# Kernel optimization log

Hardware: AMD Instinct MI355X
Metric: run time of the kernel (lower is better)

The kernel has to match this reference:

```python
import jax, jax.numpy as jnp
import numpy as np

CTX_WIN = 5
PAD = (CTX_WIN - 1) // 2


def setup_inputs() -> dict:
    key = jax.random.key(0)
    k1, k2, k3 = jax.random.split(key, 3)
    B, S, H, A = 64, 1024, 128, 8
    return {
        "batch_docIn": jax.random.normal(k1, (B, S, H), dtype=jnp.float32),
        "aspEmbed_weight": jax.random.uniform(k2, (A, CTX_WIN * H), dtype=jnp.float32, minval=-0.01, maxval=0.01),
        "aspProj": jax.random.uniform(k3, (A, H, H), dtype=jnp.float32, minval=-0.01, maxval=0.01),
    }


def reference(batch_docIn, aspEmbed_weight, aspProj):
    B, S, H = batch_docIn.shape
    A = aspProj.shape[0]
    # Per-aspect projection: (A, B, S, H)
    proj = jnp.einsum('bsh,ahf->absf', batch_docIn, aspProj)
    E = aspEmbed_weight.reshape(A, H, CTX_WIN)
    # Zero-pad along seq, then accumulate windowed scores without materializing
    padded = jnp.pad(proj, ((0, 0), (0, 0), (PAD, PAD), (0, 0)))
    attn = sum(
        jnp.einsum('absh,ah->abs',
                   jax.lax.dynamic_slice_in_dim(padded, w, S, axis=2),
                   E[:, :, w])
        for w in range(CTX_WIN)
    )  # (A, B, S)
    attn = jax.nn.softmax(attn, axis=2)  # softmax over seq (torch dim=1)
    rep = jnp.einsum('absh,abs->abh', proj, attn)  # (A, B, H)
    # outputs: attn (B, A, S), rep (B, A, H)
    return attn.transpose(1, 0, 2), rep.transpose(1, 0, 2)
```

## Files before the change

kernel.cpp:

```cpp
#include <hip/hip_runtime.h>
#include <hip/hip_bf16.h>

#define S_DIM 1024
#define H_DIM 128
#define A_DIM 8
#define W_WIN 5

typedef unsigned int uint;
typedef unsigned short ushort;
typedef __attribute__((ext_vector_type(8))) short short8;
typedef __attribute__((ext_vector_type(4))) float f32x4;

union U128 { uint4 u; short8 s; };

__device__ __forceinline__ ushort f2bf(float f) {
    uint u = __float_as_uint(f);
    uint r = (u + 0x7fffu + ((u >> 16) & 1u)) >> 16;
    return (ushort)r;
}

__global__ __launch_bounds__(128) void k_g(const float* __restrict__ P,
                                           const float* __restrict__ We,
                                           ushort* __restrict__ Gt) {
    const int a = blockIdx.x;
    const int h = threadIdx.x;
    if (a >= A_DIM) {
        for (int i = h; i < W_WIN * H_DIM; i += 128) Gt[a * (W_WIN * H_DIM) + i] = 0;
        return;
    }
    __shared__ float Es[H_DIM * W_WIN];
    for (int i = h; i < H_DIM * W_WIN; i += 128) Es[i] = We[a * (H_DIM * W_WIN) + i];
    __syncthreads();

    const float* Pr = P + ((size_t)a * H_DIM + h) * H_DIM;
    float acc[W_WIN] = {0.f, 0.f, 0.f, 0.f, 0.f};
#pragma unroll 8
    for (int f = 0; f < H_DIM; f += 4) {
        float4 pv = *(const float4*)(Pr + f);
        float pj[4] = {pv.x, pv.y, pv.z, pv.w};
#pragma unroll
        for (int j = 0; j < 4; ++j) {
            const float p = pj[j];
            const float* e = &Es[(f + j) * W_WIN];
#pragma unroll
            for (int w = 0; w < W_WIN; ++w) acc[w] += p * e[w];
        }
    }
#pragma unroll
    for (int w = 0; w < W_WIN; ++w)
        Gt[a * (W_WIN * H_DIM) + w * H_DIM + h] = f2bf(acc[w]);
}

#define CS 128
#define RROWS (CS + 4)
#define GPAD 81
#define EPITCH 136
__global__ __launch_bounds__(256) void k_scores(const float* __restrict__ Din,
                                                const ushort* __restrict__ Gt,
                                                float* __restrict__ escore,
                                                float* __restrict__ numPart,
                                                float* __restrict__ Zpart) {
    __shared__ uint4 Dl[RROWS * 16];
    __shared__ uint4 Gl[16 * GPAD];
    __shared__ ushort el[16 * EPITCH];
    __shared__ float Zw[32];
    const int b   = blockIdx.y;
    const int slc = blockIdx.x;
    const int s0  = slc * CS;
    const int t   = threadIdx.x;
    const float* Db = Din + (size_t)b * S_DIM * H_DIM;

    for (int i = t; i < RROWS * 16; i += 256) {
        const int r = i >> 4, c = i & 15;
        const int gs = s0 - 2 + r;
        float4 va = make_float4(0.f, 0.f, 0.f, 0.f), vb = va;
        if (gs >= 0 && gs < S_DIM) {
            const float* p = Db + (size_t)gs * H_DIM + c * 8;
            va = ((const float4*)p)[0];
            vb = ((const float4*)p)[1];
        }
        uint4 q;
        q.x = (uint)f2bf(va.x) | ((uint)f2bf(va.y) << 16);
        q.y = (uint)f2bf(va.z) | ((uint)f2bf(va.w) << 16);
        q.z = (uint)f2bf(vb.x) | ((uint)f2bf(vb.y) << 16);
        q.w = (uint)f2bf(vb.z) | ((uint)f2bf(vb.w) << 16);
        Dl[r * 16 + (c ^ (r & 15))] = q;
    }
    {
        const uint4* Gg = (const uint4*)Gt;
        for (int i = t; i < 16 * 80; i += 256) {
            const int n = i / 80, c = i - n * 80;
            Gl[n * GPAD + c] = Gg[i];
        }
    }
    __syncthreads();

    const int lane = t & 63;
    const int wv   = t >> 6;
    const int lm   = lane & 15;
    const int lq   = lane >> 4;

    f32x4 acc0 = {0.f, 0.f, 0.f, 0.f};
    f32x4 acc1 = {0.f, 0.f, 0.f, 0.f};
#pragma unroll
    for (int kk = 0; kk < 20; ++kk) {
        const int w = kk >> 2;
        const int r0 = wv * 16 + lm + w;
        const int cidx = (kk & 3) * 4 + lq;
        const int cx = cidx ^ (r0 & 15);
        U128 av0, av1, bv;
        bv.u  = Gl[lm * GPAD + kk * 4 + lq];
        av0.u = Dl[r0 * 16 + cx];
        av1.u = Dl[(r0 + 64) * 16 + cx];
        acc0 = __builtin_amdgcn_mfma_f32_16x16x32_bf16(av0.s, bv.s, acc0, 0, 0, 0);
        acc1 = __builtin_amdgcn_mfma_f32_16x16x32_bf16(av1.s, bv.s, acc1, 0, 0, 0);
    }

    float4 e0, e1;
    e0.x = __expf(acc0.x); e0.y = __expf(acc0.y); e0.z = __expf(acc0.z); e0.w = __expf(acc0.w);
    e1.x = __expf(acc1.x); e1.y = __expf(acc1.y); e1.z = __expf(acc1.z); e1.w = __expf(acc1.w);

    if (lm < A_DIM) {
        float* op = escore + (((size_t)b * A_DIM + lm) * S_DIM) + s0 + wv * 16 + lq * 4;
        *(float4*)op = e0;
        *(float4*)(op + 64) = e1;
    }
    {
        const int sb = wv * 16 + lq * 4;
        uint2 d0, d1;
        d0.x = (uint)f2bf(e0.x) | ((uint)f2bf(e0.y) << 16);
        d0.y = (uint)f2bf(e0.z) | ((uint)f2bf(e0.w) << 16);
        d1.x = (uint)f2bf(e1.x) | ((uint)f2bf(e1.y) << 16);
        d1.y = (uint)f2bf(e1.z) | ((uint)f2bf(e1.w) << 16);
        *(uint2*)(&el[lm * EPITCH + sb])      = d0;
        *(uint2*)(&el[lm * EPITCH + sb + 64]) = d1;
    }
    float es = e0.x + e0.y + e0.z + e0.w + e1.x + e1.y + e1.z + e1.w;
    es += __shfl_xor(es, 16);
    es += __shfl_xor(es, 32);
    if (lq == 0 && lm < A_DIM) Zw[wv * 8 + lm] = es;
    __syncthreads();

    const ushort* Dls = (const ushort*)Dl;
    U128 afr[4];
#pragma unroll
    for (int kk = 0; kk < 4; ++kk)
        afr[kk].u = *(const uint4*)(&el[lm * EPITCH + kk * 32 + lq * 8]);

    f32x4 accN[2] = {{0.f,0.f,0.f,0.f},{0.f,0.f,0.f,0.f}};
#pragma unroll
    for (int nt = 0; nt < 2; ++nt) {
        const int h  = (wv * 2 + nt) * 16 + lm;
        const int ch = h >> 3, hw = h & 7;
#pragma unroll
        for (int kk = 0; kk < 4; ++kk) {
            uint p[4];
#pragma unroll
            for (int jj = 0; jj < 4; ++jj) {
                const int sj = kk * 32 + lq * 8 + jj * 2;
                const int ra = sj + 2, rb = sj + 3;
                const uint lo = Dls[(ra * 16 + (ch ^ (ra & 15))) * 8 + hw];
                const uint hi = Dls[(rb * 16 + (ch ^ (rb & 15))) * 8 + hw];
                p[jj] = lo | (hi << 16);
            }
            U128 bfr; bfr.u = make_uint4(p[0], p[1], p[2], p[3]);
            accN[nt] = __builtin_amdgcn_mfma_f32_16x16x32_bf16(afr[kk].s, bfr.s, accN[nt], 0, 0, 0);
        }
    }

    if (lq < 2) {
#pragma unroll
        for (int nt = 0; nt < 2; ++nt) {
            const int h = (wv * 2 + nt) * 16 + lm;
#pragma unroll
            for (int r = 0; r < 4; ++r)
                numPart[(((size_t)(b * 8 + slc) * 8) + lq * 4 + r) * H_DIM + h] = accN[nt][r];
        }
    }
    if (t < A_DIM)
        Zpart[(b * 8 + slc) * 8 + t] = Zw[t] + Zw[8 + t] + Zw[16 + t] + Zw[24 + t];
}

__global__ __launch_bounds__(128) void k_final(const float* __restrict__ escore,
                                               const float* __restrict__ numPart,
                                               const float* __restrict__ Zpart,
                                               const float* __restrict__ P,
                                               float* __restrict__ attn,
                                               float* __restrict__ rep) {
    __shared__ float ws[H_DIM];
    const int ba = blockIdx.x;
    const int b = ba >> 3, a = ba & 7;
    const int t = threadIdx.x;

    float Zs = 0.f;
#pragma unroll
    for (int k = 0; k < 8; ++k) Zs += Zpart[(b * 8 + k) * 8 + a];
    const float rz = 1.0f / Zs;

    float s = 0.f;
#pragma unroll
    for (int k = 0; k < 8; ++k)
        s += numPart[(((size_t)(b * 8 + k) * 8) + a) * H_DIM + t];
    ws[t] = s * rz;

    const float* ep = escore + (size_t)ba * S_DIM;
    float* ap = attn + (size_t)ba * S_DIM;
#pragma unroll
    for (int i = 0; i < 2; ++i) {
        float4 v = *(const float4*)(ep + i * 512 + t * 4);
        v.x *= rz; v.y *= rz; v.z *= rz; v.w *= rz;
        *(float4*)(ap + i * 512 + t * 4) = v;
    }
    __syncthreads();

    const float* Pa = P + (size_t)a * H_DIM * H_DIM + t;
    float acc = 0.f;
#pragma unroll 32
    for (int hh = 0; hh < H_DIM; ++hh)
        acc += ws[hh] * Pa[(size_t)hh * H_DIM];
    rep[(size_t)ba * H_DIM + t] = acc;
}

extern "C" void kernel_launch(void* const* d_in, const int* in_sizes, int n_in,
                              void* d_out, int out_size, void* d_ws, size_t ws_size,
                              hipStream_t stream) {
    const float* docIn = (const float*)d_in[0];
    const float* We    = (const float*)d_in[1];
    const float* P     = (const float*)d_in[2];
    float* out = (float*)d_out;

    const int B = in_sizes[0] / (S_DIM * H_DIM);

    ushort* Gt     = (ushort*)d_ws;
    float* escore  = (float*)((char*)d_ws + 32768);
    float* numPart = escore + (size_t)B * A_DIM * S_DIM;
    float* Zpart   = numPart + (size_t)B * 8 * A_DIM * H_DIM;

    k_g<<<16, 128, 0, stream>>>(P, We, Gt);
    k_scores<<<dim3(S_DIM / CS, B), 256, 0, stream>>>(docIn, Gt, escore, numPart, Zpart);
    k_final<<<B * A_DIM, 128, 0, stream>>>(escore, numPart, Zpart, P, out,
                                           out + (size_t)B * A_DIM * S_DIM);
}
```

Measured before the change: 91.94 us.

## Fuse final normalization and projection into scores kernel via last-block atomics

Result: slower. 112.2 us (+22.0%).

```diff
diff --git a/kernel.cpp b/kernel.cpp
--- a/kernel.cpp
+++ b/kernel.cpp
@@ -21,9 +21,21 @@
 
 __global__ __launch_bounds__(128) void k_g(const float* __restrict__ P,
                                            const float* __restrict__ We,
-                                           ushort* __restrict__ Gt) {
+                                           ushort* __restrict__ Gt,
+                                           float* __restrict__ numAcc,
+                                           float* __restrict__ Z,
+                                           uint* __restrict__ cnt) {
     const int a = blockIdx.x;
     const int h = threadIdx.x;
+
+    {
+        float4 z4 = make_float4(0.f, 0.f, 0.f, 0.f);
+        float4* np = (float4*)(numAcc + (size_t)a * 4096);
+        for (int i = h; i < 1024; i += 128) np[i] = z4;
+        if (a == 0) for (int i = h; i < 64 * A_DIM; i += 128) Z[i] = 0.f;
+        if (a == 1 && h < 64) cnt[h] = 0u;
+    }
+
     if (a >= A_DIM) {
         for (int i = h; i < W_WIN * H_DIM; i += 128) Gt[a * (W_WIN * H_DIM) + i] = 0;
         return;
@@ -55,15 +67,20 @@
 #define RROWS (CS + 4)
 #define GPAD 81
 #define EPITCH 136
-__global__ __launch_bounds__(256) void k_scores(const float* __restrict__ Din,
-                                                const ushort* __restrict__ Gt,
-                                                float* __restrict__ escore,
-                                                float* __restrict__ numPart,
-                                                float* __restrict__ Zpart) {
+__global__ __launch_bounds__(256) void k_fused(const float* __restrict__ Din,
+                                               const ushort* __restrict__ Gt,
+                                               const float* __restrict__ P,
+                                               float* __restrict__ escore,
+                                               float* __restrict__ numAcc,
+                                               float* __restrict__ Z,
+                                               uint* __restrict__ cnt,
+                                               float* __restrict__ attn,
+                                               float* __restrict__ rep) {
     __shared__ uint4 Dl[RROWS * 16];
     __shared__ uint4 Gl[16 * GPAD];
     __shared__ ushort el[16 * EPITCH];
     __shared__ float Zw[32];
+    __shared__ int lastFlag;
     const int b   = blockIdx.y;
     const int slc = blockIdx.x;
     const int s0  = slc * CS;
@@ -174,51 +191,52 @@
             const int h = (wv * 2 + nt) * 16 + lm;
 #pragma unroll
             for (int r = 0; r < 4; ++r)
-                numPart[(((size_t)(b * 8 + slc) * 8) + lq * 4 + r) * H_DIM + h] = accN[nt][r];
+                atomicAdd(&numAcc[((size_t)(b * 8 + lq * 4 + r)) * H_DIM + h], accN[nt][r]);
         }
     }
     if (t < A_DIM)
-        Zpart[(b * 8 + slc) * 8 + t] = Zw[t] + Zw[8 + t] + Zw[16 + t] + Zw[24 + t];
-}
-
-__global__ __launch_bounds__(128) void k_final(const float* __restrict__ escore,
-                                               const float* __restrict__ numPart,
-                                               const float* __restrict__ Zpart,
-                                               const float* __restrict__ P,
-                                               float* __restrict__ attn,
-                                               float* __restrict__ rep) {
-    __shared__ float ws[H_DIM];
-    const int ba = blockIdx.x;
-    const int b = ba >> 3, a = ba & 7;
-    const int t = threadIdx.x;
-
-    float Zs = 0.f;
-#pragma unroll
-    for (int k = 0; k < 8; ++k) Zs += Zpart[(b * 8 + k) * 8 + a];
-    const float rz = 1.0f / Zs;
-
-    float s = 0.f;
-#pragma unroll
-    for (int k = 0; k < 8; ++k)
-        s += numPart[(((size_t)(b * 8 + k) * 8) + a) * H_DIM + t];
-    ws[t] = s * rz;
-
-    const float* ep = escore + (size_t)ba * S_DIM;
-    float* ap = attn + (size_t)ba * S_DIM;
-#pragma unroll
-    for (int i = 0; i < 2; ++i) {
-        float4 v = *(const float4*)(ep + i * 512 + t * 4);
+        atomicAdd(&Z[b * A_DIM + t], Zw[t] + Zw[8 + t] + Zw[16 + t] + Zw[24 + t]);
+    __syncthreads();
+
+    if (t == 0) {
+        __threadfence();
+        lastFlag = (atomicAdd(&cnt[b], 1u) == 7u);
+    }
+    __syncthreads();
+    if (!lastFlag) return;
+    __threadfence();
+
+    float* wsl = (float*)Gl;
+    float* Zf  = wsl + 1024;
+    if (t < A_DIM) Zf[t] = 1.0f / Z[b * A_DIM + t];
+    __syncthreads();
+
+#pragma unroll
+    for (int i = 0; i < 4; ++i) {
+        const int idx = t + 256 * i;
+        wsl[idx] = numAcc[(size_t)b * 8 * H_DIM + idx] * Zf[idx >> 7];
+    }
+#pragma unroll
+    for (int a = 0; a < A_DIM; ++a) {
+        const size_t off = ((size_t)b * A_DIM + a) * S_DIM + t * 4;
+        float4 v = *(const float4*)(escore + off);
+        const float rz = Zf[a];
         v.x *= rz; v.y *= rz; v.z *= rz; v.w *= rz;
-        *(float4*)(ap + i * 512 + t * 4) = v;
-    }
-    __syncthreads();
-
-    const float* Pa = P + (size_t)a * H_DIM * H_DIM + t;
-    float acc = 0.f;
+        *(float4*)(attn + off) = v;
+    }
+    __syncthreads();
+#pragma unroll
+    for (int i = 0; i < 4; ++i) {
+        const int idx = t + 256 * i;
+        const int a = idx >> 7, f = idx & 127;
+        const float* Pa = P + ((size_t)a * H_DIM) * H_DIM + f;
+        const float* wa = wsl + a * H_DIM;
+        float acc = 0.f;
 #pragma unroll 32
-    for (int hh = 0; hh < H_DIM; ++hh)
-        acc += ws[hh] * Pa[(size_t)hh * H_DIM];
-    rep[(size_t)ba * H_DIM + t] = acc;
+        for (int hh = 0; hh < H_DIM; ++hh)
+            acc += wa[hh] * Pa[(size_t)hh * H_DIM];
+        rep[(size_t)b * A_DIM * H_DIM + idx] = acc;
+    }
 }
 
 extern "C" void kernel_launch(void* const* d_in, const int* in_sizes, int n_in,
@@ -233,11 +251,12 @@
 
     ushort* Gt     = (ushort*)d_ws;
     float* escore  = (float*)((char*)d_ws + 32768);
-    float* numPart = escore + (size_t)B * A_DIM * S_DIM;
-    float* Zpart   = numPart + (size_t)B * 8 * A_DIM * H_DIM;
-
-    k_g<<<16, 128, 0, stream>>>(P, We, Gt);
-    k_scores<<<dim3(S_DIM / CS, B), 256, 0, stream>>>(docIn, Gt, escore, numPart, Zpart);
-    k_final<<<B * A_DIM, 128, 0, stream>>>(escore, numPart, Zpart, P, out,
-                                           out + (size_t)B * A_DIM * S_DIM);
-}
+    float* numAcc  = escore + (size_t)B * A_DIM * S_DIM;
+    float* Z       = numAcc + (size_t)B * A_DIM * H_DIM;
+    uint*  cnt     = (uint*)(Z + B * A_DIM);
+
+    k_g<<<16, 128, 0, stream>>>(P, We, Gt, numAcc, Z, cnt);
+    k_fused<<<dim3(S_DIM / CS, B), 256, 0, stream>>>(docIn, Gt, P, escore,
+                                                     numAcc, Z, cnt, out,
+                                                     out + (size_t)B * A_DIM * S_DIM);
+}
```

## Halve score chunk size, store exp-scores as bf16, swizzle G in LDS

Applied to the files above, without the earlier changes.

Result: no change. 92.21 us (+0.3%).

```diff
diff --git a/kernel.cpp b/kernel.cpp
--- a/kernel.cpp
+++ b/kernel.cpp
@@ -51,17 +51,16 @@
         Gt[a * (W_WIN * H_DIM) + w * H_DIM + h] = f2bf(acc[w]);
 }
 
-#define CS 128
+#define CS 64
 #define RROWS (CS + 4)
-#define GPAD 81
-#define EPITCH 136
+#define EPITCH 88
 __global__ __launch_bounds__(256) void k_scores(const float* __restrict__ Din,
                                                 const ushort* __restrict__ Gt,
-                                                float* __restrict__ escore,
+                                                ushort* __restrict__ escore,
                                                 float* __restrict__ numPart,
                                                 float* __restrict__ Zpart) {
     __shared__ uint4 Dl[RROWS * 16];
-    __shared__ uint4 Gl[16 * GPAD];
+    __shared__ uint4 Gl[16 * 80];
     __shared__ ushort el[16 * EPITCH];
     __shared__ float Zw[32];
     const int b   = blockIdx.y;
@@ -90,7 +89,7 @@
         const uint4* Gg = (const uint4*)Gt;
         for (int i = t; i < 16 * 80; i += 256) {
             const int n = i / 80, c = i - n * 80;
-            Gl[n * GPAD + c] = Gg[i];
+            Gl[n * 80 + ((c & ~15) | ((c & 15) ^ (n & 15)))] = Gg[i];
         }
     }
     __syncthreads();
@@ -101,59 +100,47 @@
     const int lq   = lane >> 4;
 
     f32x4 acc0 = {0.f, 0.f, 0.f, 0.f};
-    f32x4 acc1 = {0.f, 0.f, 0.f, 0.f};
 #pragma unroll
     for (int kk = 0; kk < 20; ++kk) {
         const int w = kk >> 2;
         const int r0 = wv * 16 + lm + w;
         const int cidx = (kk & 3) * 4 + lq;
-        const int cx = cidx ^ (r0 & 15);
-        U128 av0, av1, bv;
-        bv.u  = Gl[lm * GPAD + kk * 4 + lq];
-        av0.u = Dl[r0 * 16 + cx];
-        av1.u = Dl[(r0 + 64) * 16 + cx];
-        acc0 = __builtin_amdgcn_mfma_f32_16x16x32_bf16(av0.s, bv.s, acc0, 0, 0, 0);
-        acc1 = __builtin_amdgcn_mfma_f32_16x16x32_bf16(av1.s, bv.s, acc1, 0, 0, 0);
-    }
-
-    float4 e0, e1;
+        const int gc = kk * 4 + lq;
+        U128 av, bv;
+        bv.u = Gl[lm * 80 + ((gc & ~15) | ((gc & 15) ^ (lm & 15)))];
+        av.u = Dl[r0 * 16 + (cidx ^ (r0 & 15))];
+        acc0 = __builtin_amdgcn_mfma_f32_16x16x32_bf16(av.s, bv.s, acc0, 0, 0, 0);
+    }
+
+    float4 e0;
     e0.x = __expf(acc0.x); e0.y = __expf(acc0.y); e0.z = __expf(acc0.z); e0.w = __expf(acc0.w);
-    e1.x = __expf(acc1.x); e1.y = __expf(acc1.y); e1.z = __expf(acc1.z); e1.w = __expf(acc1.w);
-
-    if (lm < A_DIM) {
-        float* op = escore + (((size_t)b * A_DIM + lm) * S_DIM) + s0 + wv * 16 + lq * 4;
-        *(float4*)op = e0;
-        *(float4*)(op + 64) = e1;
-    }
-    {
-        const int sb = wv * 16 + lq * 4;
-        uint2 d0, d1;
-        d0.x = (uint)f2bf(e0.x) | ((uint)f2bf(e0.y) << 16);
-        d0.y = (uint)f2bf(e0.z) | ((uint)f2bf(e0.w) << 16);
-        d1.x = (uint)f2bf(e1.x) | ((uint)f2bf(e1.y) << 16);
-        d1.y = (uint)f2bf(e1.z) | ((uint)f2bf(e1.w) << 16);
-        *(uint2*)(&el[lm * EPITCH + sb])      = d0;
-        *(uint2*)(&el[lm * EPITCH + sb + 64]) = d1;
-    }
-    float es = e0.x + e0.y + e0.z + e0.w + e1.x + e1.y + e1.z + e1.w;
+    uint2 d0;
+    d0.x = (uint)f2bf(e0.x) | ((uint)f2bf(e0.y) << 16);
+    d0.y = (uint)f2bf(e0.z) | ((uint)f2bf(e0.w) << 16);
+    const int sb = wv * 16 + lq * 4;
+    if (lm < A_DIM)
+        *(uint2*)(escore + (((size_t)b * A_DIM + lm) << 10) + s0 + sb) = d0;
+    *(uint2*)(&el[lm * EPITCH + sb]) = d0;
+
+    float es = e0.x + e0.y + e0.z + e0.w;
     es += __shfl_xor(es, 16);
     es += __shfl_xor(es, 32);
     if (lq == 0 && lm < A_DIM) Zw[wv * 8 + lm] = es;
     __syncthreads();
 
     const ushort* Dls = (const ushort*)Dl;
-    U128 afr[4];
-#pragma unroll
-    for (int kk = 0; kk < 4; ++kk)
+    U128 afr[2];
+#pragma unroll
+    for (int kk = 0; kk < 2; ++kk)
         afr[kk].u = *(const uint4*)(&el[lm * EPITCH + kk * 32 + lq * 8]);
 
     f32x4 accN[2] = {{0.f,0.f,0.f,0.f},{0.f,0.f,0.f,0.f}};
 #pragma unroll
     for (int nt = 0; nt < 2; ++nt) {
-        const int h  = (wv * 2 + nt) * 16 + lm;
+        const int h  = wv * 32 + nt * 16 + lm;
         const int ch = h >> 3, hw = h & 7;
 #pragma unroll
-        for (int kk = 0; kk < 4; ++kk) {
+        for (int kk = 0; kk < 2; ++kk) {
             uint p[4];
 #pragma unroll
             for (int jj = 0; jj < 4; ++jj) {
@@ -171,17 +158,17 @@
     if (lq < 2) {
 #pragma unroll
         for (int nt = 0; nt < 2; ++nt) {
-            const int h = (wv * 2 + nt) * 16 + lm;
+            const int h = wv * 32 + nt * 16 + lm;
 #pragma unroll
             for (int r = 0; r < 4; ++r)
-                numPart[(((size_t)(b * 8 + slc) * 8) + lq * 4 + r) * H_DIM + h] = accN[nt][r];
+                numPart[(((size_t)(b * 16 + slc) * 8) + lq * 4 + r) * H_DIM + h] = accN[nt][r];
         }
     }
     if (t < A_DIM)
-        Zpart[(b * 8 + slc) * 8 + t] = Zw[t] + Zw[8 + t] + Zw[16 + t] + Zw[24 + t];
-}
-
-__global__ __launch_bounds__(128) void k_final(const float* __restrict__ escore,
+        Zpart[(b * 16 + slc) * 8 + t] = Zw[t] + Zw[8 + t] + Zw[16 + t] + Zw[24 + t];
+}
+
+__global__ __launch_bounds__(128) void k_final(const ushort* __restrict__ escore,
                                                const float* __restrict__ numPart,
                                                const float* __restrict__ Zpart,
                                                const float* __restrict__ P,
@@ -194,21 +181,25 @@
 
     float Zs = 0.f;
 #pragma unroll
-    for (int k = 0; k < 8; ++k) Zs += Zpart[(b * 8 + k) * 8 + a];
+    for (int k = 0; k < 16; ++k) Zs += Zpart[(b * 16 + k) * 8 + a];
     const float rz = 1.0f / Zs;
 
     float s = 0.f;
 #pragma unroll
-    for (int k = 0; k < 8; ++k)
-        s += numPart[(((size_t)(b * 8 + k) * 8) + a) * H_DIM + t];
+    for (int k = 0; k < 16; ++k)
+        s += numPart[(((size_t)(b * 16 + k) * 8) + a) * H_DIM + t];
     ws[t] = s * rz;
 
-    const float* ep = escore + (size_t)ba * S_DIM;
+    const ushort* ep = escore + (size_t)ba * S_DIM;
     float* ap = attn + (size_t)ba * S_DIM;
 #pragma unroll
     for (int i = 0; i < 2; ++i) {
-        float4 v = *(const float4*)(ep + i * 512 + t * 4);
-        v.x *= rz; v.y *= rz; v.z *= rz; v.w *= rz;
+        uint2 q = *(const uint2*)(ep + i * 512 + t * 4);
+        float4 v;
+        v.x = __uint_as_float(q.x << 16) * rz;
+        v.y = __uint_as_float(q.x & 0xffff0000u) * rz;
+        v.z = __uint_as_float(q.y << 16) * rz;
+        v.w = __uint_as_float(q.y & 0xffff0000u) * rz;
         *(float4*)(ap + i * 512 + t * 4) = v;
     }
     __syncthreads();
@@ -232,9 +223,10 @@
     const int B = in_sizes[0] / (S_DIM * H_DIM);
 
     ushort* Gt     = (ushort*)d_ws;
-    float* escore  = (float*)((char*)d_ws + 32768);
-    float* numPart = escore + (size_t)B * A_DIM * S_DIM;
-    float* Zpart   = numPart + (size_t)B * 8 * A_DIM * H_DIM;
+    ushort* escore = (ushort*)((char*)d_ws + 32768);
+    float* numPart = (float*)((char*)d_ws + 32768 +
+                              (size_t)B * A_DIM * S_DIM * 2);
+    float* Zpart   = numPart + (size_t)B * 16 * 8 * H_DIM;
 
     k_g<<<16, 128, 0, stream>>>(P, We, Gt);
     k_scores<<<dim3(S_DIM / CS, B), 256, 0, stream>>>(docIn, Gt, escore, numPart, Zpart);
```
